# Optimization experiments

Measured on AMD Instinct MI355X. Metric: run time of the kernel, lower is better.

Reference implementation:

```python
import jax, jax.numpy as jnp
import numpy as np

N = 100000
E = 1600000
F_IN = 64
ACT = 8
NEG_SLOPE = 0.2


def _p(key, shape, scale=0.1):
    return jax.random.normal(key, shape, dtype=jnp.float32) * scale


def setup_inputs() -> dict:
    key = jax.random.key(0)
    ks = jax.random.split(key, 20)
    x = jax.random.normal(ks[0], (N, F_IN), dtype=jnp.float32)
    edge_index = jax.random.randint(ks[1], (2, E), 0, N, dtype=jnp.int64)
    edge_attr = jax.random.normal(ks[2], (E, 2), dtype=jnp.float32)
    # conv1: in=64, heads=4, out=16 -> 64
    H1, C1 = 4, 16
    Wl1 = _p(ks[3], (F_IN, H1 * C1)); bl1 = jnp.zeros((H1 * C1,), jnp.float32)
    Wr1 = _p(ks[4], (F_IN, H1 * C1)); br1 = jnp.zeros((H1 * C1,), jnp.float32)
    We1 = _p(ks[5], (2, H1 * C1))
    att1 = _p(ks[6], (H1, C1))
    b1 = jnp.zeros((H1 * C1,), jnp.float32)
    # conv2: in=64, heads=2, out=32 -> 64
    H2, C2 = 2, 32
    Wl2 = _p(ks[7], (H1 * C1, H2 * C2)); bl2 = jnp.zeros((H2 * C2,), jnp.float32)
    Wr2 = _p(ks[8], (H1 * C1, H2 * C2)); br2 = jnp.zeros((H2 * C2,), jnp.float32)
    We2 = _p(ks[9], (2, H2 * C2))
    att2 = _p(ks[10], (H2, C2))
    b2 = jnp.zeros((H2 * C2,), jnp.float32)
    Wm = _p(ks[11], (H2 * C2, ACT)); bm = jnp.zeros((ACT,), jnp.float32)
    return dict(x=x, edge_index=edge_index, edge_attr=edge_attr,
                Wl1=Wl1, bl1=bl1, Wr1=Wr1, br1=br1, We1=We1, att1=att1, b1=b1,
                Wl2=Wl2, bl2=bl2, Wr2=Wr2, br2=br2, We2=We2, att2=att2, b2=b2,
                Wm=Wm, bm=bm)


def gatv2_layer(x, src, dst, ea, Wl, bl, Wr, br, We, att, b, n_nodes, heads, ch):
    """PyG GATv2Conv with concat=True, add_self_loops=True (fill_value='mean')."""
    # self loops: edge attr = mean of incoming edge attrs per node (0 if none)
    deg = jax.ops.segment_sum(jnp.ones((src.shape[0],), ea.dtype), dst, n_nodes)
    loop_attr = jax.ops.segment_sum(ea, dst, n_nodes) / jnp.maximum(deg, 1.0)[:, None]
    loop = jnp.arange(n_nodes, dtype=src.dtype)
    s = jnp.concatenate([src, loop]); d = jnp.concatenate([dst, loop])
    ea_full = jnp.concatenate([ea, loop_attr], axis=0)
    xl = (x @ Wl + bl).reshape(n_nodes, heads, ch)   # source transform
    xr = (x @ Wr + br).reshape(n_nodes, heads, ch)   # target transform
    ee = (ea_full @ We).reshape(-1, heads, ch)
    e = jax.nn.leaky_relu(xl[s] + xr[d] + ee, NEG_SLOPE)  # [E', H, C]
    logits = jnp.einsum('ehc,hc->eh', e, att)             # [E', H]
    # segment softmax over destination (every node has a self loop -> non-empty)
    m = jax.ops.segment_max(logits, d, n_nodes)
    expl = jnp.exp(logits - m[d])
    denom = jax.ops.segment_sum(expl, d, n_nodes)
    alpha = expl / (denom[d] + 1e-16)
    out = jax.ops.segment_sum(xl[s] * alpha[:, :, None], d, n_nodes)
    return out.reshape(n_nodes, heads * ch) + b


def reference(x, edge_index, edge_attr, Wl1, bl1, Wr1, br1, We1, att1, b1,
              Wl2, bl2, Wr2, br2, We2, att2, b2, Wm, bm):
    src, dst = edge_index[0], edge_index[1]
    h = jax.nn.relu(gatv2_layer(x, src, dst, edge_attr, Wl1, bl1, Wr1, br1,
                                We1, att1, b1, N, 4, 16))
    h = jax.nn.relu(gatv2_layer(h, src, dst, edge_attr, Wl2, bl2, Wr2, br2,
                                We2, att2, b2, N, 2, 32))
    return jnp.tanh(h @ Wm + bm)
```

## Files before the change

### kernel.cpp

```cpp
#include <hip/hip_runtime.h>
#include <hip/hip_bf16.h>


constexpr int CAP = 64;

static __device__ __forceinline__ float bf2f(__hip_bfloat16 v) { return __bfloat162float(v); }
static __device__ __forceinline__ float bits2f(unsigned int u) { return __uint_as_float(u << 16); }
static __device__ __forceinline__ unsigned int f2bfbits(float f) {
  unsigned int u = __float_as_uint(f);
  return ((u + 0x7FFFu + ((u >> 16) & 1u)) >> 16) & 0xFFFFu;
}
static __device__ __forceinline__ float bcast(float v, int k) {
  return __int_as_float(__builtin_amdgcn_readlane(__float_as_int(v), k));
}

template <int CTRL>
static __device__ __forceinline__ float dpp_add(float v) {
  int m = __builtin_amdgcn_update_dpp(0, __float_as_int(v), CTRL, 0xf, 0xf, false);
  return v + __int_as_float(m);
}
static __device__ __forceinline__ float row16_sum(float p) {
  p = dpp_add<0x128>(p);
  p = dpp_add<0x124>(p);
  p = dpp_add<0x122>(p);
  p = dpp_add<0x121>(p);
  return p;
}
template <int C>
static __device__ __forceinline__ float head_sum(float p) {
  p = row16_sum(p);
  if (C == 32) p += __shfl_xor(p, 16);
  return p;
}
static __device__ __forceinline__ float wave64_sum(float p) {
  p = row16_sum(p);
  p += __shfl_xor(p, 16);
  p += __shfl_xor(p, 32);
  return p;
}

template <typename T> static __device__ __forceinline__ float ldv(const T* p, size_t i);
template <> __device__ __forceinline__ float ldv<float>(const float* p, size_t i) { return p[i]; }
template <> __device__ __forceinline__ float ldv<__hip_bfloat16>(const __hip_bfloat16* p, size_t i) {
  return bf2f(p[i]);
}
template <typename T> static __device__ __forceinline__ void stv(T* p, size_t i, float v);
template <> __device__ __forceinline__ void stv<float>(float* p, size_t i, float v) { p[i] = v; }
template <> __device__ __forceinline__ void stv<__hip_bfloat16>(__hip_bfloat16* p, size_t i,
                                                                float v) {
  p[i] = __float2bfloat16(v);
}

__global__ void k_count(const int* __restrict__ dst, int* __restrict__ cnt, int E, int N) {
  int i = blockIdx.x * 256 + threadIdx.x;
  if (i >= E) return;
  int d = dst[i]; d = min(max(d, 0), N - 1);
  atomicAdd(&cnt[d], 1);
}

__global__ __launch_bounds__(1024) void k_scan_local(const int* __restrict__ deg,
                                                     int* __restrict__ off,
                                                     int* __restrict__ bsum, int n) {
  __shared__ int s[1024];
  int t = threadIdx.x;
  int g = blockIdx.x * 1024 + t;
  int v = (g < n) ? deg[g] : 0;
  s[t] = v;
  __syncthreads();
  for (int o = 1; o < 1024; o <<= 1) {
    int add = (t >= o) ? s[t - o] : 0;
    __syncthreads();
    s[t] += add;
    __syncthreads();
  }
  if (g < n) off[g] = s[t] - v;
  if (t == 1023) bsum[blockIdx.x] = s[t];
}

__global__ __launch_bounds__(256) void k_scan_part(const int* __restrict__ bsum,
                                                   int* __restrict__ boff,
                                                   int* __restrict__ off, int nb, int n) {
  __shared__ int s[256];
  int t = threadIdx.x;
  int v = (t < nb) ? bsum[t] : 0;
  s[t] = v;
  __syncthreads();
  for (int o = 1; o < 256; o <<= 1) {
    int add = (t >= o) ? s[t - o] : 0;
    __syncthreads();
    s[t] += add;
    __syncthreads();
  }
  if (t < nb) boff[t] = s[t] - v;
  if (t == nb - 1) off[n] = s[t];
}

__global__ __launch_bounds__(1024) void k_scan_add(int* __restrict__ off, int* __restrict__ cursor,
                                                   const int* __restrict__ boff, int n) {
  int g = blockIdx.x * 1024 + threadIdx.x;
  if (g < n) {
    int v = off[g] + boff[blockIdx.x];
    off[g] = v;
    cursor[g] = v;
  }
}

template <bool BUCKET>
__global__ void k_scatter(const int* __restrict__ src, const int* __restrict__ dst,
                          const float* __restrict__ ea, int* __restrict__ cursor,
                          long long* __restrict__ csr, int E, int N) {
  int i = blockIdx.x * 256 + threadIdx.x;
  if (i >= E) return;
  int d = dst[i]; d = min(max(d, 0), N - 1);
  int s = src[i]; s = min(max(s, 0), N - 1);
  unsigned int ep = f2bfbits(ea[2 * i]) | (f2bfbits(ea[2 * i + 1]) << 16);
  long long rec = (long long)(unsigned int)s | ((long long)ep << 32);
  int slot = atomicAdd(&cursor[d], 1);
  if (BUCKET) {
    if (slot < CAP) __builtin_nontemporal_store(rec, &csr[(long long)d * CAP + slot]);
  } else {
    __builtin_nontemporal_store(rec, &csr[slot]);
  }
}

template <typename TIN, typename TOUT>
__global__ __launch_bounds__(256) void k_gemm_xlxr(const TIN* __restrict__ in,
                                                   const float* __restrict__ Wl,
                                                   const float* __restrict__ bl,
                                                   const float* __restrict__ Wr,
                                                   const float* __restrict__ br,
                                                   TOUT* __restrict__ xl,
                                                   TOUT* __restrict__ xr, int n) {
  int lane = threadIdx.x & 63, wave = threadIdx.x >> 6;
  float wl[64], wr[64];
#pragma unroll
  for (int k = 0; k < 64; ++k) {
    wl[k] = Wl[k * 64 + lane];
    wr[k] = Wr[k * 64 + lane];
  }
  float blc = bl[lane], brc = br[lane];
  const int stride = gridDim.x * 4;
  int node = blockIdx.x * 4 + wave;
  if (node >= n) return;
  float xv = ldv(in, (size_t)node * 64 + lane);
  while (node < n) {
    int nxt = node + stride;
    float xn = (nxt < n) ? ldv(in, (size_t)nxt * 64 + lane) : 0.f;
    float accl = blc, accr = brc;
#pragma unroll
    for (int k = 0; k < 64; ++k) {
      float s = bcast(xv, k);
      accl = fmaf(s, wl[k], accl);
      accr = fmaf(s, wr[k], accr);
    }
    stv(xl, (size_t)node * 64 + lane, accl);
    stv(xr, (size_t)node * 64 + lane, accr);
    node = nxt;
    xv = xn;
  }
}

template <int C, bool FUSE_MLP, bool BUCKET, typename ST>
__global__ __launch_bounds__(256) void k_agg(const ST* __restrict__ xl,
                                             const ST* __restrict__ xr,
                                             const long long* __restrict__ csr,
                                             const int* __restrict__ off,
                                             const int* __restrict__ cnt,
                                             const float* __restrict__ We,
                                             const float* __restrict__ att,
                                             const float* __restrict__ b,
                                             const float* __restrict__ Wm,
                                             const float* __restrict__ bm,
                                             ST* __restrict__ hout,
                                             float* __restrict__ fout, int n) {
  int wid = (int)((blockIdx.x * blockDim.x + threadIdx.x) >> 6);
  int lane = threadIdx.x & 63;
  if (wid >= n) return;
  const int node = __builtin_amdgcn_readfirstlane(wid);

  float xr_c = ldv(xr, (size_t)node * 64 + lane);
  float xl_self = ldv(xl, (size_t)node * 64 + lane);
  float We0 = We[lane];
  float We1 = We[64 + lane];
  float attc = att[lane];
  float bc = b[lane];

  int dg, start, end;
  if (BUCKET) {
    dg = cnt[node];
    start = node * CAP;
    end = start + min(dg, CAP);
  } else {
    start = off[node];
    end = off[node + 1];
    dg = end - start;
  }

  float den0 = 0.f, num0 = 0.f, den1 = 0.f, num1 = 0.f;
  float ea0acc = 0.f, ea1acc = 0.f;

  for (int base = start; base < end; base += 64) {
    int c64 = min(64, end - base);
    long long meta = (lane < c64) ? __builtin_nontemporal_load(&csr[base + lane]) : 0LL;
    int mlo = (int)(unsigned long long)meta;
    int mhi = (int)((unsigned long long)meta >> 32);
    ea0acc += bits2f((unsigned)mhi & 0xffffu);
    ea1acc += bits2f((unsigned)mhi >> 16);

    constexpr int G = 4;
    float xs[G];
    unsigned eps[G];
    int npre = min(G, c64);
#pragma unroll
    for (int g = 0; g < G; ++g)
      if (g < npre) {
        int s = __builtin_amdgcn_readlane(mlo, g);
        eps[g] = (unsigned)__builtin_amdgcn_readlane(mhi, g);
        xs[g] = ldv(xl, (size_t)s * 64 + lane);
      }
    for (int t = 0; t < c64; t += G) {
      int cur = min(G, c64 - t);
      float xc[G];
      unsigned epc[G];
#pragma unroll
      for (int g = 0; g < G; ++g) {
        xc[g] = xs[g];
        epc[g] = eps[g];
      }
      int nt = t + G;
      int nn = min(G, c64 - nt);
#pragma unroll
      for (int g = 0; g < G; ++g)
        if (g < nn) {
          int s = __builtin_amdgcn_readlane(mlo, nt + g);
          eps[g] = (unsigned)__builtin_amdgcn_readlane(mhi, nt + g);
          xs[g] = ldv(xl, (size_t)s * 64 + lane);
        }
#pragma unroll
      for (int g = 0; g < G; ++g)
        if (g < cur) {
          float ea0 = bits2f(epc[g] & 0xffffu);
          float ea1 = bits2f(epc[g] >> 16);
          float e = xc[g] + xr_c;
          e = fmaf(ea0, We0, e);
          e = fmaf(ea1, We1, e);
          e = fmaxf(e, 0.2f * e);
          float p = head_sum<C>(e * attc);
          float ex = __expf(p);
          if (g & 1) {
            den1 += ex;
            num1 = fmaf(ex, xc[g], num1);
          } else {
            den0 += ex;
            num0 = fmaf(ex, xc[g], num0);
          }
        }
    }
  }
  float den = den0 + den1, num = num0 + num1;

  {
    float s0 = wave64_sum(ea0acc);
    float s1 = wave64_sum(ea1acc);
    float inv = 1.0f / (float)max(dg, 1);
    float e = xl_self + xr_c;
    e = fmaf(s0 * inv, We0, e);
    e = fmaf(s1 * inv, We1, e);
    e = fmaxf(e, 0.2f * e);
    float p = head_sum<C>(e * attc);
    float ex = __expf(p);
    den += ex;
    num = fmaf(ex, xl_self, num);
  }

  float o = num / (den + 1e-16f) + bc;
  o = fmaxf(o, 0.f);

  if (!FUSE_MLP) {
    stv(hout, (size_t)node * 64 + lane, o);
  } else {
    float wm[8];
#pragma unroll
    for (int j = 0; j < 8; ++j) wm[j] = Wm[lane * 8 + j];
    float mine = 0.f;
#pragma unroll
    for (int j = 0; j < 8; ++j) {
      float p = wave64_sum(o * wm[j]);
      if (lane == j) mine = p;
    }
    if (lane < 8) fout[(size_t)node * 8 + lane] = tanhf(mine + bm[lane]);
  }
}

extern "C" void kernel_launch(void* const* d_in, const int* in_sizes, int n_in,
                              void* d_out, int out_size, void* d_ws, size_t ws_size,
                              hipStream_t stream) {
  const float* x = (const float*)d_in[0];
  const int* ei = (const int*)d_in[1];
  const float* ea = (const float*)d_in[2];
  const float* Wl1 = (const float*)d_in[3];
  const float* bl1 = (const float*)d_in[4];
  const float* Wr1 = (const float*)d_in[5];
  const float* br1 = (const float*)d_in[6];
  const float* We1 = (const float*)d_in[7];
  const float* att1 = (const float*)d_in[8];
  const float* b1 = (const float*)d_in[9];
  const float* Wl2 = (const float*)d_in[10];
  const float* bl2 = (const float*)d_in[11];
  const float* Wr2 = (const float*)d_in[12];
  const float* br2 = (const float*)d_in[13];
  const float* We2 = (const float*)d_in[14];
  const float* att2 = (const float*)d_in[15];
  const float* b2 = (const float*)d_in[16];
  const float* Wm = (const float*)d_in[17];
  const float* bm = (const float*)d_in[18];
  float* out = (float*)d_out;

  const int N = in_sizes[0] / 64;
  const int E = in_sizes[1] / 2;
  const int* src = ei;
  const int* dst = ei + E;

  auto al = [](size_t x) { return (x + 255) & ~(size_t)255; };
  const size_t needA_f32 = al((size_t)N * 4) + al((size_t)N * CAP * 8) + 3 * al((size_t)N * 64 * 4);
  const size_t fixedB = al((size_t)N * 4) + al((size_t)(N + 1) * 4) + al((size_t)N * 4) +
                        al(1024) + al(1024) + al((size_t)E * 8);
  const size_t needB_f32 = fixedB + 3 * al((size_t)N * 64 * 4);

  char* p = (char*)d_ws;
  auto alloc = [&](size_t bytes) {
    char* r = p;
    p += (bytes + 255) & ~(size_t)255;
    return r;
  };

  const int egrid = (E + 255) / 256;
  const int agrid = (N + 3) / 4;
  const int ggrid = 1024;
  const int NB = (N + 1023) / 1024;

  if (ws_size >= needA_f32) {
    int* cnt = (int*)alloc((size_t)N * 4);
    long long* csr = (long long*)alloc((size_t)N * CAP * 8);
    float* xl = (float*)alloc((size_t)N * 64 * 4);
    float* xr = (float*)alloc((size_t)N * 64 * 4);
    float* h = (float*)alloc((size_t)N * 64 * 4);

    hipMemsetAsync(cnt, 0, (size_t)N * 4, stream);
    k_scatter<true><<<egrid, 256, 0, stream>>>(src, dst, ea, cnt, csr, E, N);

    k_gemm_xlxr<float, float><<<ggrid, 256, 0, stream>>>(x, Wl1, bl1, Wr1, br1, xl, xr, N);
    k_agg<16, false, true, float><<<agrid, 256, 0, stream>>>(
        xl, xr, csr, nullptr, cnt, We1, att1, b1, nullptr, nullptr, h, nullptr, N);
    k_gemm_xlxr<float, float><<<ggrid, 256, 0, stream>>>(h, Wl2, bl2, Wr2, br2, xl, xr, N);
    k_agg<32, true, true, float><<<agrid, 256, 0, stream>>>(
        xl, xr, csr, nullptr, cnt, We2, att2, b2, Wm, bm, nullptr, out, N);
  } else {
    bool f32s = ws_size >= needB_f32;
    int* cnt = (int*)alloc((size_t)N * 4);
    int* off = (int*)alloc((size_t)(N + 1) * 4);
    int* cursor = (int*)alloc((size_t)N * 4);
    int* bsum = (int*)alloc(1024);
    int* boff = (int*)alloc(1024);
    long long* csr = (long long*)alloc((size_t)E * 8);
    size_t ssz = f32s ? 4 : 2;
    void* xlv = alloc((size_t)N * 64 * ssz);
    void* xrv = alloc((size_t)N * 64 * ssz);
    void* hv = alloc((size_t)N * 64 * ssz);

    hipMemsetAsync(cnt, 0, (size_t)N * 4, stream);
    k_count<<<egrid, 256, 0, stream>>>(dst, cnt, E, N);
    k_scan_local<<<NB, 1024, 0, stream>>>(cnt, off, bsum, N);
    k_scan_part<<<1, 256, 0, stream>>>(bsum, boff, off, NB, N);
    k_scan_add<<<NB, 1024, 0, stream>>>(off, cursor, boff, N);
    k_scatter<false><<<egrid, 256, 0, stream>>>(src, dst, ea, cursor, csr, E, N);

    if (f32s) {
      float* xl = (float*)xlv;
      float* xr = (float*)xrv;
      float* h = (float*)hv;
      k_gemm_xlxr<float, float><<<ggrid, 256, 0, stream>>>(x, Wl1, bl1, Wr1, br1, xl, xr, N);
      k_agg<16, false, false, float><<<agrid, 256, 0, stream>>>(
          xl, xr, csr, off, nullptr, We1, att1, b1, nullptr, nullptr, h, nullptr, N);
      k_gemm_xlxr<float, float><<<ggrid, 256, 0, stream>>>(h, Wl2, bl2, Wr2, br2, xl, xr, N);
      k_agg<32, true, false, float><<<agrid, 256, 0, stream>>>(
          xl, xr, csr, off, nullptr, We2, att2, b2, Wm, bm, nullptr, out, N);
    } else {
      __hip_bfloat16* xl = (__hip_bfloat16*)xlv;
      __hip_bfloat16* xr = (__hip_bfloat16*)xrv;
      __hip_bfloat16* h = (__hip_bfloat16*)hv;
      k_gemm_xlxr<float, __hip_bfloat16><<<ggrid, 256, 0, stream>>>(x, Wl1, bl1, Wr1, br1, xl, xr,
                                                                    N);
      k_agg<16, false, false, __hip_bfloat16><<<agrid, 256, 0, stream>>>(
          xl, xr, csr, off, nullptr, We1, att1, b1, nullptr, nullptr, h, nullptr, N);
      k_gemm_xlxr<__hip_bfloat16, __hip_bfloat16><<<ggrid, 256, 0, stream>>>(h, Wl2, bl2, Wr2, br2,
                                                                             xl, xr, N);
      k_agg<32, true, false, __hip_bfloat16><<<agrid, 256, 0, stream>>>(
          xl, xr, csr, off, nullptr, We2, att2, b2, Wm, bm, nullptr, out, N);
    }
  }
}
```

Measured before the change: 539.3 us.

## Process four edges per wave with float4 gathers in aggregation; vectorize scatter

The fp32 aggregation kernel is restructured so each wave splits into four 16-lane groups. Each group handles a different edge with float4 loads of the source row, and the partial softmax sums are combined across groups at the end. This cuts the serial per-edge loop length and widens the gather loads to raise memory-level parallelism. The edge scatter kernel now processes four edges per thread with vector loads of src, dst and edge attributes, and the bf16 path keeps a simplified scalar aggregation kernel. The trade-off is extra cross-lane reductions and masked work on partial tail groups.

```diff
diff --git a/kernel.cpp b/kernel.cpp
--- a/kernel.cpp
+++ b/kernel.cpp
@@ -26,10 +26,9 @@
   p = dpp_add<0x121>(p);
   return p;
 }
-template <int C>
-static __device__ __forceinline__ float head_sum(float p) {
-  p = row16_sum(p);
-  if (C == 32) p += __shfl_xor(p, 16);
+static __device__ __forceinline__ float quad_sum(float p) {
+  p = dpp_add<0xB1>(p);
+  p = dpp_add<0x4E>(p);
   return p;
 }
 static __device__ __forceinline__ float wave64_sum(float p) {
@@ -109,17 +108,50 @@
 __global__ void k_scatter(const int* __restrict__ src, const int* __restrict__ dst,
                           const float* __restrict__ ea, int* __restrict__ cursor,
                           long long* __restrict__ csr, int E, int N) {
-  int i = blockIdx.x * 256 + threadIdx.x;
-  if (i >= E) return;
-  int d = dst[i]; d = min(max(d, 0), N - 1);
-  int s = src[i]; s = min(max(s, 0), N - 1);
-  unsigned int ep = f2bfbits(ea[2 * i]) | (f2bfbits(ea[2 * i + 1]) << 16);
-  long long rec = (long long)(unsigned int)s | ((long long)ep << 32);
-  int slot = atomicAdd(&cursor[d], 1);
-  if (BUCKET) {
-    if (slot < CAP) __builtin_nontemporal_store(rec, &csr[(long long)d * CAP + slot]);
+  int i0 = (blockIdx.x * 256 + threadIdx.x) * 4;
+  if (i0 >= E) return;
+  if (i0 + 4 <= E) {
+    int4 sv = *(const int4*)(src + i0);
+    int4 dv = *(const int4*)(dst + i0);
+    float4 ea01 = *(const float4*)(ea + 2 * i0);
+    float4 ea23 = *(const float4*)(ea + 2 * i0 + 4);
+    int ss[4] = {sv.x, sv.y, sv.z, sv.w};
+    int dd[4] = {dv.x, dv.y, dv.z, dv.w};
+    float e0[4] = {ea01.x, ea01.z, ea23.x, ea23.z};
+    float e1[4] = {ea01.y, ea01.w, ea23.y, ea23.w};
+    long long rec[4];
+    int slot[4], d[4];
+#pragma unroll
+    for (int j = 0; j < 4; ++j) {
+      d[j] = min(max(dd[j], 0), N - 1);
+      int s = min(max(ss[j], 0), N - 1);
+      unsigned int ep = f2bfbits(e0[j]) | (f2bfbits(e1[j]) << 16);
+      rec[j] = (long long)(unsigned int)s | ((long long)ep << 32);
+    }
+#pragma unroll
+    for (int j = 0; j < 4; ++j) slot[j] = atomicAdd(&cursor[d[j]], 1);
+#pragma unroll
+    for (int j = 0; j < 4; ++j) {
+      if (BUCKET) {
+        if (slot[j] < CAP)
+          __builtin_nontemporal_store(rec[j], &csr[(long long)d[j] * CAP + slot[j]]);
+      } else {
+        __builtin_nontemporal_store(rec[j], &csr[slot[j]]);
+      }
+    }
   } else {
-    __builtin_nontemporal_store(rec, &csr[slot]);
+    for (int i = i0; i < E; ++i) {
+      int d = min(max(dst[i], 0), N - 1);
+      int s = min(max(src[i], 0), N - 1);
+      unsigned int ep = f2bfbits(ea[2 * i]) | (f2bfbits(ea[2 * i + 1]) << 16);
+      long long rec = (long long)(unsigned int)s | ((long long)ep << 32);
+      int slot = atomicAdd(&cursor[d], 1);
+      if (BUCKET) {
+        if (slot < CAP) __builtin_nontemporal_store(rec, &csr[(long long)d * CAP + slot]);
+      } else {
+        __builtin_nontemporal_store(rec, &csr[slot]);
+      }
+    }
   }
 }
 
@@ -160,30 +192,33 @@
   }
 }
 
-template <int C, bool FUSE_MLP, bool BUCKET, typename ST>
-__global__ __launch_bounds__(256) void k_agg(const ST* __restrict__ xl,
-                                             const ST* __restrict__ xr,
-                                             const long long* __restrict__ csr,
-                                             const int* __restrict__ off,
-                                             const int* __restrict__ cnt,
-                                             const float* __restrict__ We,
-                                             const float* __restrict__ att,
-                                             const float* __restrict__ b,
-                                             const float* __restrict__ Wm,
-                                             const float* __restrict__ bm,
-                                             ST* __restrict__ hout,
-                                             float* __restrict__ fout, int n) {
+template <int C, bool FUSE_MLP, bool BUCKET>
+__global__ __launch_bounds__(256) void k_agg4(const float* __restrict__ xl,
+                                              const float* __restrict__ xr,
+                                              const long long* __restrict__ csr,
+                                              const int* __restrict__ off,
+                                              const int* __restrict__ cnt,
+                                              const float* __restrict__ We,
+                                              const float* __restrict__ att,
+                                              const float* __restrict__ b,
+                                              const float* __restrict__ Wm,
+                                              const float* __restrict__ bm,
+                                              float* __restrict__ hout,
+                                              float* __restrict__ fout, int n) {
   int wid = (int)((blockIdx.x * blockDim.x + threadIdx.x) >> 6);
   int lane = threadIdx.x & 63;
   if (wid >= n) return;
   const int node = __builtin_amdgcn_readfirstlane(wid);
-
-  float xr_c = ldv(xr, (size_t)node * 64 + lane);
-  float xl_self = ldv(xl, (size_t)node * 64 + lane);
-  float We0 = We[lane];
-  float We1 = We[64 + lane];
-  float attc = att[lane];
-  float bc = b[lane];
+  const int sub = lane & 15;
+  const int grp = lane >> 4;
+  const int grp4 = grp << 2;
+
+  float4 xr4 = ((const float4*)(xr + (size_t)node * 64))[sub];
+  float4 xls4 = ((const float4*)(xl + (size_t)node * 64))[sub];
+  float4 We04 = ((const float4*)We)[sub];
+  float4 We14 = ((const float4*)(We + 64))[sub];
+  float4 att4 = ((const float4*)att)[sub];
+  float4 b4 = ((const float4*)b)[sub];
 
   int dg, start, end;
   if (BUCKET) {
@@ -196,7 +231,8 @@
     dg = end - start;
   }
 
-  float den0 = 0.f, num0 = 0.f, den1 = 0.f, num1 = 0.f;
+  float den = 0.f;
+  float4 num = {0.f, 0.f, 0.f, 0.f};
   float ea0acc = 0.f, ea1acc = 0.f;
 
   for (int base = start; base < end; base += 64) {
@@ -204,88 +240,187 @@
     long long meta = (lane < c64) ? __builtin_nontemporal_load(&csr[base + lane]) : 0LL;
     int mlo = (int)(unsigned long long)meta;
     int mhi = (int)((unsigned long long)meta >> 32);
-    ea0acc += bits2f((unsigned)mhi & 0xffffu);
-    ea1acc += bits2f((unsigned)mhi >> 16);
-
-    constexpr int G = 4;
-    float xs[G];
-    unsigned eps[G];
-    int npre = min(G, c64);
-#pragma unroll
-    for (int g = 0; g < G; ++g)
-      if (g < npre) {
-        int s = __builtin_amdgcn_readlane(mlo, g);
-        eps[g] = (unsigned)__builtin_amdgcn_readlane(mhi, g);
-        xs[g] = ldv(xl, (size_t)s * 64 + lane);
+    ea0acc += __uint_as_float((unsigned)mhi << 16);
+    ea1acc += __uint_as_float((unsigned)mhi & 0xffff0000u);
+
+    int iters = (c64 + 3) >> 2;
+    int se0 = __builtin_amdgcn_ds_bpermute(grp4, mlo);
+    int ep0 = __builtin_amdgcn_ds_bpermute(grp4, mhi);
+    float4 xg0 = ((const float4*)(xl + (size_t)(unsigned)se0 * 64))[sub];
+    for (int t = 0; t < iters; ++t) {
+      int se1 = 0, ep1 = 0;
+      float4 xg1 = {0.f, 0.f, 0.f, 0.f};
+      if (t + 1 < iters) {
+        int idx = ((t + 1) << 4) + grp4;
+        se1 = __builtin_amdgcn_ds_bpermute(idx, mlo);
+        ep1 = __builtin_amdgcn_ds_bpermute(idx, mhi);
+        xg1 = ((const float4*)(xl + (size_t)(unsigned)se1 * 64))[sub];
       }
-    for (int t = 0; t < c64; t += G) {
-      int cur = min(G, c64 - t);
-      float xc[G];
-      unsigned epc[G];
-#pragma unroll
-      for (int g = 0; g < G; ++g) {
-        xc[g] = xs[g];
-        epc[g] = eps[g];
-      }
-      int nt = t + G;
-      int nn = min(G, c64 - nt);
-#pragma unroll
-      for (int g = 0; g < G; ++g)
-        if (g < nn) {
-          int s = __builtin_amdgcn_readlane(mlo, nt + g);
-          eps[g] = (unsigned)__builtin_amdgcn_readlane(mhi, nt + g);
-          xs[g] = ldv(xl, (size_t)s * 64 + lane);
-        }
-#pragma unroll
-      for (int g = 0; g < G; ++g)
-        if (g < cur) {
-          float ea0 = bits2f(epc[g] & 0xffffu);
-          float ea1 = bits2f(epc[g] >> 16);
-          float e = xc[g] + xr_c;
-          e = fmaf(ea0, We0, e);
-          e = fmaf(ea1, We1, e);
-          e = fmaxf(e, 0.2f * e);
-          float p = head_sum<C>(e * attc);
-          float ex = __expf(p);
-          if (g & 1) {
-            den1 += ex;
-            num1 = fmaf(ex, xc[g], num1);
-          } else {
-            den0 += ex;
-            num0 = fmaf(ex, xc[g], num0);
-          }
-        }
-    }
-  }
-  float den = den0 + den1, num = num0 + num1;
+      float ea0 = __uint_as_float((unsigned)ep0 << 16);
+      float ea1 = __uint_as_float((unsigned)ep0 & 0xffff0000u);
+      float4 e;
+      e.x = fmaf(ea1, We14.x, fmaf(ea0, We04.x, xg0.x + xr4.x));
+      e.y = fmaf(ea1, We14.y, fmaf(ea0, We04.y, xg0.y + xr4.y));
+      e.z = fmaf(ea1, We14.z, fmaf(ea0, We04.z, xg0.z + xr4.z));
+      e.w = fmaf(ea1, We14.w, fmaf(ea0, We04.w, xg0.w + xr4.w));
+      e.x = fmaxf(e.x, 0.2f * e.x);
+      e.y = fmaxf(e.y, 0.2f * e.y);
+      e.z = fmaxf(e.z, 0.2f * e.z);
+      e.w = fmaxf(e.w, 0.2f * e.w);
+      float p = e.x * att4.x;
+      p = fmaf(e.y, att4.y, p);
+      p = fmaf(e.z, att4.z, p);
+      p = fmaf(e.w, att4.w, p);
+      p = quad_sum(p);
+      if (C == 32) p += __shfl_xor(p, 4);
+      bool valid = ((t << 2) + grp) < c64;
+      float ex = valid ? __expf(p) : 0.f;
+      den += ex;
+      num.x = fmaf(ex, xg0.x, num.x);
+      num.y = fmaf(ex, xg0.y, num.y);
+      num.z = fmaf(ex, xg0.z, num.z);
+      num.w = fmaf(ex, xg0.w, num.w);
+      se0 = se1; ep0 = ep1; xg0 = xg1;
+    }
+  }
+
+  den += __shfl_xor(den, 16);
+  den += __shfl_xor(den, 32);
+  num.x += __shfl_xor(num.x, 16); num.x += __shfl_xor(num.x, 32);
+  num.y += __shfl_xor(num.y, 16); num.y += __shfl_xor(num.y, 32);
+  num.z += __shfl_xor(num.z, 16); num.z += __shfl_xor(num.z, 32);
+  num.w += __shfl_xor(num.w, 16); num.w += __shfl_xor(num.w, 32);
 
   {
     float s0 = wave64_sum(ea0acc);
     float s1 = wave64_sum(ea1acc);
     float inv = 1.0f / (float)max(dg, 1);
-    float e = xl_self + xr_c;
-    e = fmaf(s0 * inv, We0, e);
-    e = fmaf(s1 * inv, We1, e);
+    float a0 = s0 * inv, a1 = s1 * inv;
+    float4 e;
+    e.x = fmaf(a1, We14.x, fmaf(a0, We04.x, xls4.x + xr4.x));
+    e.y = fmaf(a1, We14.y, fmaf(a0, We04.y, xls4.y + xr4.y));
+    e.z = fmaf(a1, We14.z, fmaf(a0, We04.z, xls4.z + xr4.z));
+    e.w = fmaf(a1, We14.w, fmaf(a0, We04.w, xls4.w + xr4.w));
+    e.x = fmaxf(e.x, 0.2f * e.x);
+    e.y = fmaxf(e.y, 0.2f * e.y);
+    e.z = fmaxf(e.z, 0.2f * e.z);
+    e.w = fmaxf(e.w, 0.2f * e.w);
+    float p = e.x * att4.x;
+    p = fmaf(e.y, att4.y, p);
+    p = fmaf(e.z, att4.z, p);
+    p = fmaf(e.w, att4.w, p);
+    p = quad_sum(p);
+    if (C == 32) p += __shfl_xor(p, 4);
+    float ex = __expf(p);
+    den += ex;
+    num.x = fmaf(ex, xls4.x, num.x);
+    num.y = fmaf(ex, xls4.y, num.y);
+    num.z = fmaf(ex, xls4.z, num.z);
+    num.w = fmaf(ex, xls4.w, num.w);
+  }
+
+  float inv = 1.0f / (den + 1e-16f);
+  float4 o;
+  o.x = fmaxf(fmaf(num.x, inv, b4.x), 0.f);
+  o.y = fmaxf(fmaf(num.y, inv, b4.y), 0.f);
+  o.z = fmaxf(fmaf(num.z, inv, b4.z), 0.f);
+  o.w = fmaxf(fmaf(num.w, inv, b4.w), 0.f);
+
+  if (!FUSE_MLP) {
+    if (grp == 0) ((float4*)(hout + (size_t)node * 64))[sub] = o;
+  } else {
+    float4 wr0a = *(const float4*)(Wm + (4 * sub + 0) * 8);
+    float4 wr0b = *(const float4*)(Wm + (4 * sub + 0) * 8 + 4);
+    float4 wr1a = *(const float4*)(Wm + (4 * sub + 1) * 8);
+    float4 wr1b = *(const float4*)(Wm + (4 * sub + 1) * 8 + 4);
+    float4 wr2a = *(const float4*)(Wm + (4 * sub + 2) * 8);
+    float4 wr2b = *(const float4*)(Wm + (4 * sub + 2) * 8 + 4);
+    float4 wr3a = *(const float4*)(Wm + (4 * sub + 3) * 8);
+    float4 wr3b = *(const float4*)(Wm + (4 * sub + 3) * 8 + 4);
+    const float* w0 = (const float*)&wr0a;
+    const float* w0h = (const float*)&wr0b;
+    const float* w1 = (const float*)&wr1a;
+    const float* w1h = (const float*)&wr1b;
+    const float* w2 = (const float*)&wr2a;
+    const float* w2h = (const float*)&wr2b;
+    const float* w3 = (const float*)&wr3a;
+    const float* w3h = (const float*)&wr3b;
+    float mine = 0.f;
+#pragma unroll
+    for (int j = 0; j < 8; ++j) {
+      float c0 = (j < 4) ? w0[j & 3] : w0h[j & 3];
+      float c1 = (j < 4) ? w1[j & 3] : w1h[j & 3];
+      float c2 = (j < 4) ? w2[j & 3] : w2h[j & 3];
+      float c3 = (j < 4) ? w3[j & 3] : w3h[j & 3];
+      float p = o.x * c0;
+      p = fmaf(o.y, c1, p);
+      p = fmaf(o.z, c2, p);
+      p = fmaf(o.w, c3, p);
+      p = row16_sum(p);
+      if (lane == j) mine = p;
+    }
+    if (lane < 8) fout[(size_t)node * 8 + lane] = tanhf(mine + bm[lane]);
+  }
+}
+
+template <int C, bool FUSE_MLP, typename ST>
+__global__ __launch_bounds__(256) void k_agg(const ST* __restrict__ xl, const ST* __restrict__ xr,
+                                             const long long* __restrict__ csr,
+                                             const int* __restrict__ off,
+                                             const float* __restrict__ We,
+                                             const float* __restrict__ att,
+                                             const float* __restrict__ b,
+                                             const float* __restrict__ Wm,
+                                             const float* __restrict__ bm, ST* __restrict__ hout,
+                                             float* __restrict__ fout, int n) {
+  int wid = (int)((blockIdx.x * blockDim.x + threadIdx.x) >> 6);
+  int lane = threadIdx.x & 63;
+  if (wid >= n) return;
+  const int node = __builtin_amdgcn_readfirstlane(wid);
+  float xr_c = ldv(xr, (size_t)node * 64 + lane);
+  float xl_self = ldv(xl, (size_t)node * 64 + lane);
+  float We0 = We[lane], We1 = We[64 + lane], attc = att[lane], bc = b[lane];
+  int start = off[node], end = off[node + 1], dg = end - start;
+  float den = 0.f, num = 0.f, ea0acc = 0.f, ea1acc = 0.f;
+  for (int base = start; base < end; base += 64) {
+    int c64 = min(64, end - base);
+    long long meta = (lane < c64) ? csr[base + lane] : 0;
+    int mlo = (int)(unsigned long long)meta;
+    int mhi = (int)((unsigned long long)meta >> 32);
+    ea0acc += bits2f((unsigned)mhi & 0xffffu);
+    ea1acc += bits2f((unsigned)mhi >> 16);
+    for (int t = 0; t < c64; ++t) {
+      int s = __builtin_amdgcn_readlane(mlo, t);
+      unsigned ep = (unsigned)__builtin_amdgcn_readlane(mhi, t);
+      float xls = ldv(xl, (size_t)s * 64 + lane);
+      float e = xls + xr_c + bits2f(ep & 0xffffu) * We0 + bits2f(ep >> 16) * We1;
+      e = fmaxf(e, 0.2f * e);
+      float p = row16_sum(e * attc);
+      if (C == 32) p += __shfl_xor(p, 16);
+      float ex = __expf(p);
+      den += ex;
+      num = fmaf(ex, xls, num);
+    }
+  }
+  {
+    float s0 = wave64_sum(ea0acc), s1 = wave64_sum(ea1acc);
+    float inv = 1.0f / (float)max(dg, 1);
+    float e = xl_self + xr_c + s0 * inv * We0 + s1 * inv * We1;
     e = fmaxf(e, 0.2f * e);
-    float p = head_sum<C>(e * attc);
+    float p = row16_sum(e * attc);
+    if (C == 32) p += __shfl_xor(p, 16);
     float ex = __expf(p);
     den += ex;
     num = fmaf(ex, xl_self, num);
   }
-
-  float o = num / (den + 1e-16f) + bc;
-  o = fmaxf(o, 0.f);
-
+  float o = fmaxf(num / (den + 1e-16f) + bc, 0.f);
   if (!FUSE_MLP) {
     stv(hout, (size_t)node * 64 + lane, o);
   } else {
-    float wm[8];
-#pragma unroll
-    for (int j = 0; j < 8; ++j) wm[j] = Wm[lane * 8 + j];
     float mine = 0.f;
 #pragma unroll
     for (int j = 0; j < 8; ++j) {
-      float p = wave64_sum(o * wm[j]);
+      float p = wave64_sum(o * Wm[lane * 8 + j]);
       if (lane == j) mine = p;
     }
     if (lane < 8) fout[(size_t)node * 8 + lane] = tanhf(mine + bm[lane]);
@@ -334,6 +469,7 @@
     return r;
   };
 
+  const int egrid4 = (E + 1023) / 1024;
   const int egrid = (E + 255) / 256;
   const int agrid = (N + 3) / 4;
   const int ggrid = 1024;
@@ -347,14 +483,14 @@
     float* h = (float*)alloc((size_t)N * 64 * 4);
 
     hipMemsetAsync(cnt, 0, (size_t)N * 4, stream);
-    k_scatter<true><<<egrid, 256, 0, stream>>>(src, dst, ea, cnt, csr, E, N);
+    k_scatter<true><<<egrid4, 256, 0, stream>>>(src, dst, ea, cnt, csr, E, N);
 
     k_gemm_xlxr<float, float><<<ggrid, 256, 0, stream>>>(x, Wl1, bl1, Wr1, br1, xl, xr, N);
-    k_agg<16, false, true, float><<<agrid, 256, 0, stream>>>(
-        xl, xr, csr, nullptr, cnt, We1, att1, b1, nullptr, nullptr, h, nullptr, N);
+    k_agg4<16, false, true><<<agrid, 256, 0, stream>>>(xl, xr, csr, nullptr, cnt, We1, att1, b1,
+                                                       nullptr, nullptr, h, nullptr, N);
     k_gemm_xlxr<float, float><<<ggrid, 256, 0, stream>>>(h, Wl2, bl2, Wr2, br2, xl, xr, N);
-    k_agg<32, true, true, float><<<agrid, 256, 0, stream>>>(
-        xl, xr, csr, nullptr, cnt, We2, att2, b2, Wm, bm, nullptr, out, N);
+    k_agg4<32, true, true><<<agrid, 256, 0, stream>>>(xl, xr, csr, nullptr, cnt, We2, att2, b2,
+                                                      Wm, bm, nullptr, out, N);
   } else {
     bool f32s = ws_size >= needB_f32;
     int* cnt = (int*)alloc((size_t)N * 4);
@@ -373,30 +509,30 @@
     k_scan_local<<<NB, 1024, 0, stream>>>(cnt, off, bsum, N);
     k_scan_part<<<1, 256, 0, stream>>>(bsum, boff, off, NB, N);
     k_scan_add<<<NB, 1024, 0, stream>>>(off, cursor, boff, N);
-    k_scatter<false><<<egrid, 256, 0, stream>>>(src, dst, ea, cursor, csr, E, N);
+    k_scatter<false><<<egrid4, 256, 0, stream>>>(src, dst, ea, cursor, csr, E, N);
 
     if (f32s) {
       float* xl = (float*)xlv;
       float* xr = (float*)xrv;
       float* h = (float*)hv;
       k_gemm_xlxr<float, float><<<ggrid, 256, 0, stream>>>(x, Wl1, bl1, Wr1, br1, xl, xr, N);
-      k_agg<16, false, false, float><<<agrid, 256, 0, stream>>>(
-          xl, xr, csr, off, nullptr, We1, att1, b1, nullptr, nullptr, h, nullptr, N);
+      k_agg4<16, false, false><<<agrid, 256, 0, stream>>>(xl, xr, csr, off, nullptr, We1, att1,
+                                                          b1, nullptr, nullptr, h, nullptr, N);
       k_gemm_xlxr<float, float><<<ggrid, 256, 0, stream>>>(h, Wl2, bl2, Wr2, br2, xl, xr, N);
-      k_agg<32, true, false, float><<<agrid, 256, 0, stream>>>(
-          xl, xr, csr, off, nullptr, We2, att2, b2, Wm, bm, nullptr, out, N);
+      k_agg4<32, true, false><<<agrid, 256, 0, stream>>>(xl, xr, csr, off, nullptr, We2, att2, b2,
+                                                         Wm, bm, nullptr, out, N);
     } else {
       __hip_bfloat16* xl = (__hip_bfloat16*)xlv;
       __hip_bfloat16* xr = (__hip_bfloat16*)xrv;
       __hip_bfloat16* h = (__hip_bfloat16*)hv;
       k_gemm_xlxr<float, __hip_bfloat16><<<ggrid, 256, 0, stream>>>(x, Wl1, bl1, Wr1, br1, xl, xr,
                                                                     N);
-      k_agg<16, false, false, __hip_bfloat16><<<agrid, 256, 0, stream>>>(
-          xl, xr, csr, off, nullptr, We1, att1, b1, nullptr, nullptr, h, nullptr, N);
+      k_agg<16, false, __hip_bfloat16><<<agrid, 256, 0, stream>>>(
+          xl, xr, csr, off, We1, att1, b1, nullptr, nullptr, h, nullptr, N);
       k_gemm_xlxr<__hip_bfloat16, __hip_bfloat16><<<ggrid, 256, 0, stream>>>(h, Wl2, bl2, Wr2, br2,
                                                                              xl, xr, N);
-      k_agg<32, true, false, __hip_bfloat16><<<agrid, 256, 0, stream>>>(
-          xl, xr, csr, off, nullptr, We2, att2, b2, Wm, bm, nullptr, out, N);
-    }
-  }
-}
+      k_agg<32, true, __hip_bfloat16><<<agrid, 256, 0, stream>>>(
+          xl, xr, csr, off, We2, att2, b2, Wm, bm, nullptr, out, N);
+    }
+  }
+}
```

New measurement: 527.3 us. -2.2%, faster.
